# Performance work log

Hardware: AMD Instinct MI355X
Metric: run time of the kernel (lower is better)

The kernel has to match this reference:

```python
import jax, jax.numpy as jnp
import numpy as np

B_, DIM, HEADS, RES = 2, 288, 12, 32
# per-branch (D_sp, H_sp, W_sp) from idx permutation of split_size=[2,2,4]
WINS = ((2, 2, 4), (2, 2, 4), (2, 4, 2))
POS_DIM = ((DIM // 3) // 4) // 4  # = 6
HB = HEADS // 3  # heads per branch = 4


def _rel_tables(Dsp, Hsp, Wsp):
    d = np.arange(1 - Dsp, Dsp); h = np.arange(1 - Hsp, Hsp); w = np.arange(1 - Wsp, Wsp)
    biases = np.stack(np.meshgrid(d, h, w, indexing='ij')).reshape(3, -1).T.astype(np.float32)
    c = np.stack(np.meshgrid(np.arange(Dsp), np.arange(Hsp), np.arange(Wsp), indexing='ij')).reshape(3, -1)
    rel = (c[:, :, None] - c[:, None, :]).transpose(1, 2, 0).astype(np.int64)
    rel[..., 0] += Dsp - 1; rel[..., 1] += Hsp - 1; rel[..., 2] += Wsp - 1
    rel[..., 0] *= (2 * Hsp - 1) * (2 * Wsp - 1); rel[..., 1] *= 2 * Wsp - 1
    return biases, rel.sum(-1).astype(np.int32)


def _ln(x, g, b):
    m = x.mean(-1, keepdims=True)
    v = jnp.mean((x - m) ** 2, axis=-1, keepdims=True)
    return (x - m) * jax.lax.rsqrt(v + 1e-5) * g + b


def setup_inputs() -> dict:
    key = jax.random.key(0)
    ks = jax.random.split(key, 10)
    C, P, L = DIM, POS_DIM, RES ** 3
    s = 0.02
    x = jax.random.normal(ks[0], (B_, L, C), jnp.float32)
    w_qkv = jax.random.normal(ks[1], (C, 3 * C), jnp.float32) * s
    w_proj = jax.random.normal(ks[2], (C, C), jnp.float32) * s
    b_proj = jnp.zeros((C,), jnp.float32)
    conv_w = jax.random.normal(ks[3], (C, 1, 3, 3, 3), jnp.float32) * s  # depthwise OIDHW
    conv_b = jnp.zeros((C,), jnp.float32)
    pos_proj_w = jax.random.normal(ks[4], (3, 3, P), jnp.float32) * s
    pos_proj_b = jnp.zeros((3, P), jnp.float32)
    ln1_g = jnp.ones((3, P)); ln1_b = jnp.zeros((3, P))
    lin1_w = jax.random.normal(ks[5], (3, P, P), jnp.float32) * s; lin1_b = jnp.zeros((3, P))
    ln2_g = jnp.ones((3, P)); ln2_b = jnp.zeros((3, P))
    lin2_w = jax.random.normal(ks[6], (3, P, P), jnp.float32) * s; lin2_b = jnp.zeros((3, P))
    ln3_g = jnp.ones((3, P)); ln3_b = jnp.zeros((3, P))
    lin3_w = jax.random.normal(ks[7], (3, P, HB), jnp.float32) * s; lin3_b = jnp.zeros((3, HB))
    tabs = [_rel_tables(*w) for w in WINS]
    rpe_biases = jnp.asarray(np.stack([t[0] for t in tabs]))  # (3, 63, 3)
    rel_index = jnp.asarray(np.stack([t[1] for t in tabs]))   # (3, 16, 16)
    return {'x': x, 'D': RES, 'H': RES, 'W': RES, 'w_qkv': w_qkv, 'w_proj': w_proj,
            'b_proj': b_proj, 'conv_w': conv_w, 'conv_b': conv_b,
            'pos_proj_w': pos_proj_w, 'pos_proj_b': pos_proj_b,
            'ln1_g': ln1_g, 'ln1_b': ln1_b, 'lin1_w': lin1_w, 'lin1_b': lin1_b,
            'ln2_g': ln2_g, 'ln2_b': ln2_b, 'lin2_w': lin2_w, 'lin2_b': lin2_b,
            'ln3_g': ln3_g, 'ln3_b': ln3_b, 'lin3_w': lin3_w, 'lin3_b': lin3_b,
            'rpe_biases': rpe_biases, 'rel_index': rel_index}


def reference(x, D, H, W, w_qkv, w_proj, b_proj, conv_w, conv_b,
              pos_proj_w, pos_proj_b, ln1_g, ln1_b, lin1_w, lin1_b,
              ln2_g, ln2_b, lin2_w, lin2_b, ln3_g, ln3_b, lin3_w, lin3_b,
              rpe_biases, rel_index):
    B, L, C = x.shape
    C3 = C // 3
    hd = C3 // HB
    scale = hd ** -0.5
    qkv = (x @ w_qkv).reshape(B, L, 3, C).transpose(2, 0, 1, 3)  # (3, B, L, C)
    outs = []
    for bi, (Dsp, Hsp, Wsp) in enumerate(WINS):
        N = Dsp * Hsp * Wsp
        lo, hi = bi * C3, (bi + 1) * C3

        def to_win(t):
            # (B, L, C3) -> windows (B', HB, N, hd)
            t = t.reshape(B, D // Dsp, Dsp, H // Hsp, Hsp, W // Wsp, Wsp, C3)
            t = t.transpose(0, 1, 3, 5, 2, 4, 6, 7).reshape(-1, N, HB, hd)
            return t.transpose(0, 2, 1, 3)

        q = to_win(qkv[0, :, :, lo:hi]) * scale
        k = to_win(qkv[1, :, :, lo:hi])
        v = to_win(qkv[2, :, :, lo:hi])
        # dynamic relative position bias MLP (residual=False path)
        p = rpe_biases[bi] @ pos_proj_w[bi] + pos_proj_b[bi]
        p = jax.nn.relu(_ln(p, ln1_g[bi], ln1_b[bi])) @ lin1_w[bi] + lin1_b[bi]
        p = jax.nn.relu(_ln(p, ln2_g[bi], ln2_b[bi])) @ lin2_w[bi] + lin2_b[bi]
        p = jax.nn.relu(_ln(p, ln3_g[bi], ln3_b[bi])) @ lin3_w[bi] + lin3_b[bi]  # (T, HB)
        bias = p[rel_index[bi].reshape(-1)].reshape(N, N, HB).transpose(2, 0, 1)  # (HB, N, N)
        attn = jax.nn.softmax(jnp.einsum('whnd,whmd->whnm', q, k) + bias[None], axis=-1)
        o = jnp.einsum('whnm,whmd->whnd', attn, v)
        o = o.transpose(0, 2, 1, 3).reshape(B, D // Dsp, H // Hsp, W // Wsp, Dsp, Hsp, Wsp, C3)
        o = o.transpose(0, 1, 4, 2, 5, 3, 6, 7).reshape(B, D, H, W, C3)
        outs.append(o)
    att = jnp.concatenate(outs, axis=-1).reshape(B, L, C)
    # locally-enhanced branch: depthwise 3x3x3 conv over v
    vimg = qkv[2].reshape(B, D, H, W, C).transpose(0, 4, 1, 2, 3)
    lcm = jax.lax.conv_general_dilated(vimg, conv_w, (1, 1, 1), 'SAME',
                                       dimension_numbers=('NCDHW', 'OIDHW', 'NCDHW'),
                                       feature_group_count=C)
    lcm = (lcm + conv_b[None, :, None, None, None]).transpose(0, 2, 3, 4, 1).reshape(B, L, C)
    return (att + lcm) @ w_proj + b_proj
```

## Files before the change

### kernel.cpp

```cpp
#include <hip/hip_runtime.h>
#include <hip/hip_bf16.h>
#include <math.h>

#define BATCH 2
#define RES   32
#define LTOK  32768
#define CDIM  288
#define NQKV  864
#define MROWS 65536

typedef unsigned short u16;
typedef u16   u16x4 __attribute__((ext_vector_type(4)));
typedef short s16x8 __attribute__((ext_vector_type(8)));
typedef float f32x4 __attribute__((ext_vector_type(4)));

__device__ __forceinline__ u16 f2bf(float f) {
  union { __hip_bfloat16 h; u16 u; } x;
  x.h = __float2bfloat16(f);
  return x.u;
}
__device__ __forceinline__ float bf2f(u16 u) {
  union { u16 u; __hip_bfloat16 h; } x;
  x.u = u;
  return __bfloat162float(x.h);
}
__device__ __forceinline__ float bflo(unsigned u) {
  union { unsigned u; float f; } x; x.u = u << 16; return x.f;
}
__device__ __forceinline__ float bfhi(unsigned u) {
  union { unsigned u; float f; } x; x.u = u & 0xffff0000u; return x.f;
}

#define ASYNC16(gsrc, ldst)                                                        \
  __builtin_amdgcn_global_load_lds(                                                \
      (const __attribute__((address_space(1))) void*)(gsrc),                       \
      (__attribute__((address_space(3))) void*)(ldst), 16, 0, 0)

__global__ __launch_bounds__(256) void transpose_cvt(
    const float* __restrict__ w, u16* __restrict__ wt, int K, int N) {
  int o = blockIdx.x * 256 + threadIdx.x;
  if (o >= N * K) return;
  int n = o / K, k = o - n * K;
  wt[o] = f2bf(w[(size_t)k * N + n]);
}

__global__ __launch_bounds__(256) void conv_w_kmajor(
    const float* __restrict__ cw, float* __restrict__ wck) {
  int o = blockIdx.x * 256 + threadIdx.x;
  if (o >= 27 * 288) return;
  int k = o / 288, c = o - k * 288;
  wck[o] = cw[c * 27 + k];
}

template <bool BF16OUT, bool ABF16>
__global__ __launch_bounds__(512) void gemm_stream(
    const void* __restrict__ Ax, const u16* __restrict__ Bt,
    const float* __restrict__ bias, void* __restrict__ out, int N) {
  __shared__ __align__(16) u16 lds[36864];
  const int bm = blockIdx.x * 64;
  const int tid = threadIdx.x;
  const int lane = tid & 63, wave = tid >> 6;
  const int m16 = lane & 15, kq = lane >> 4;
  const int wm = (wave >> 1) * 16, wn = (wave & 1) * 16;
  const int NC = N >> 5;

  if (ABF16) {
    const u16* Ab = (const u16*)Ax;
    for (int g = wave; g < 36; g += 8)
      ASYNC16(Ab + (size_t)(bm + lane) * 288 + g * 8, &lds[g * 512]);
  } else {
    const float* Af = (const float*)Ax;
#pragma unroll
    for (int p = 0; p < 9; p++) {
      int s = p * 512 + tid;
      int g2 = s >> 7, r2 = (s & 127) >> 1, half = s & 1;
      float4 v = *(const float4*)(Af + (size_t)(bm + r2) * 288 + g2 * 8 + half * 4);
      u16x4 pk;
      pk[0] = f2bf(v.x); pk[1] = f2bf(v.y); pk[2] = f2bf(v.z); pk[3] = f2bf(v.w);
      *(u16x4*)&lds[g2 * 512 + r2 * 8 + half * 4] = pk;
    }
  }
  {
    const int r = lane & 31, gh = lane >> 5;
    for (int gp = wave; gp < 18; gp += 8)
      ASYNC16(Bt + (size_t)r * 288 + (gp * 2 + gh) * 8, &lds[18432 + gp * 512]);
  }
  asm volatile("s_waitcnt vmcnt(0) lgkmcnt(0)" ::: "memory");
  __builtin_amdgcn_s_barrier();

  int buf = 0;
  for (int c = 0; c < NC; c++) {
    if (c + 1 < NC) {
      const u16* Bc = Bt + (size_t)(c + 1) * 32 * 288;
      const int r = lane & 31, gh = lane >> 5;
      const int bb0 = 18432 + (buf ^ 1) * 9216;
      for (int gp = wave; gp < 18; gp += 8)
        ASYNC16(Bc + (size_t)r * 288 + (gp * 2 + gh) * 8, &lds[bb0 + gp * 512]);
    }
    __builtin_amdgcn_sched_barrier(0);

    f32x4 acc = {0.f, 0.f, 0.f, 0.f};
    const u16* bb = &lds[18432 + buf * 9216];
#pragma unroll
    for (int ks = 0; ks < 9; ks++) {
      const int g = ks * 4 + kq;
      s16x8 af = *(const s16x8*)&lds[g * 512 + (wm + m16) * 8];
      s16x8 bf = *(const s16x8*)&bb[g * 256 + (wn + m16) * 8];
      acc = __builtin_amdgcn_mfma_f32_16x16x32_bf16(af, bf, acc, 0, 0, 0);
    }
    const int col = (c << 5) + wn + m16;
    const size_t r0 = (size_t)(bm + wm + kq * 4);
    if (BF16OUT) {
      u16* op = (u16*)out;
#pragma unroll
      for (int r = 0; r < 4; r++) op[(r0 + r) * N + col] = f2bf(acc[r]);
    } else {
      const float bv = bias ? bias[col] : 0.f;
      float* op = (float*)out;
#pragma unroll
      for (int r = 0; r < 4; r++) op[(r0 + r) * N + col] = acc[r] + bv;
    }
    if (c + 1 < NC) {
      asm volatile("s_waitcnt vmcnt(4)" ::: "memory");
      __builtin_amdgcn_s_barrier();
    }
    buf ^= 1;
  }
}

__device__ __forceinline__ void ln_relu6(const float* x, float* o,
                                         const float* g, const float* b) {
  float m = 0.f;
#pragma unroll
  for (int i = 0; i < 6; i++) m += x[i];
  m *= (1.f / 6.f);
  float v = 0.f;
#pragma unroll
  for (int i = 0; i < 6; i++) { float d = x[i] - m; v += d * d; }
  v *= (1.f / 6.f);
  float r = rsqrtf(v + 1e-5f);
#pragma unroll
  for (int i = 0; i < 6; i++) {
    float t = (x[i] - m) * r * g[i] + b[i];
    o[i] = t > 0.f ? t : 0.f;
  }
}

__global__ __launch_bounds__(256) void rpe_mlp(
    const float* __restrict__ rpe, const float* __restrict__ pw, const float* __restrict__ pb,
    const float* __restrict__ g1, const float* __restrict__ b1,
    const float* __restrict__ w1, const float* __restrict__ bb1,
    const float* __restrict__ g2, const float* __restrict__ b2,
    const float* __restrict__ w2, const float* __restrict__ bb2,
    const float* __restrict__ g3, const float* __restrict__ b3,
    const float* __restrict__ w3, const float* __restrict__ bb3,
    float* __restrict__ ptab) {
  int t = blockIdx.x * blockDim.x + threadIdx.x;
  if (t >= 3 * 63) return;
  int bi = t / 63, row = t % 63;
  float p[6], q[6];
#pragma unroll
  for (int j = 0; j < 6; j++) {
    float s = pb[bi * 6 + j];
#pragma unroll
    for (int i = 0; i < 3; i++) s += rpe[(bi * 63 + row) * 3 + i] * pw[(bi * 3 + i) * 6 + j];
    p[j] = s;
  }
  ln_relu6(p, q, g1 + bi * 6, b1 + bi * 6);
#pragma unroll
  for (int j = 0; j < 6; j++) {
    float s = bb1[bi * 6 + j];
#pragma unroll
    for (int i = 0; i < 6; i++) s += q[i] * w1[(bi * 6 + i) * 6 + j];
    p[j] = s;
  }
  ln_relu6(p, q, g2 + bi * 6, b2 + bi * 6);
#pragma unroll
  for (int j = 0; j < 6; j++) {
    float s = bb2[bi * 6 + j];
#pragma unroll
    for (int i = 0; i < 6; i++) s += q[i] * w2[(bi * 6 + i) * 6 + j];
    p[j] = s;
  }
  ln_relu6(p, q, g3 + bi * 6, b3 + bi * 6);
#pragma unroll
  for (int h = 0; h < 4; h++) {
    float s = bb3[bi * 4 + h];
#pragma unroll
    for (int i = 0; i < 6; i++) s += q[i] * w3[(bi * 6 + i) * 4 + h];
    ptab[(bi * 63 + row) * 4 + h] = s;
  }
}

__global__ __launch_bounds__(64) void attn_kernel(
    const u16* __restrict__ qkv, const float* __restrict__ ptab,
    const int* __restrict__ rel, float* __restrict__ y) {
  const int bi = blockIdx.y;
  const int wsh = (bi == 2) ? 1 : 2;
  const int hsh = (bi == 2) ? 2 : 1;
  const int Wm1 = (1 << wsh) - 1, Hm1 = (1 << hsh) - 1;
  const int nW = RES >> wsh, nH = RES >> hsh;
  const int wid = blockIdx.x;
  const int b = wid >> 11;
  const int r_ = wid & 2047;
  const int w0 = r_ % nW;
  const int r2 = r_ / nW;
  const int h0 = r2 % nH;
  const int d0 = r2 / nH;

  __shared__ __align__(16) u16 sq[16 * 40];
  __shared__ __align__(16) u16 sk[16 * 40];
  __shared__ __align__(16) u16 svt[32 * 40];
  __shared__ __align__(16) u16 sps[16 * 40];

  const int lane = threadIdx.x;
  const int m16 = lane & 15, q4 = lane >> 4;

  {
    uint4 z = make_uint4(0u, 0u, 0u, 0u);
#pragma unroll
    for (int i = lane; i < 80; i += 64) {
      *(uint4*)&sq[i * 8] = z;
      *(uint4*)&sk[i * 8] = z;
    }
#pragma unroll
    for (int i = lane; i < 160; i += 64)
      *(uint4*)&svt[i * 8] = z;
  }
  __syncthreads();

  int rv[4];
#pragma unroll
  for (int r = 0; r < 4; r++) rv[r] = rel[(bi * 16 + q4 * 4 + r) * 16 + m16];

  size_t ybase[4];
#pragma unroll
  for (int r = 0; r < 4; r++) {
    int n = q4 * 4 + r;
    int dd = n >> 3, hh2 = (n >> wsh) & Hm1, ww = n & Wm1;
    int l = ((d0 * 2 + dd) * RES + ((h0 << hsh) + hh2)) * RES + ((w0 << wsh) + ww);
    ybase[r] = (size_t)(b * LTOK + l) * CDIM + bi * 96;
  }

  const float scale = 0.20412414523193154f;

  for (int hd = 0; hd < 4; hd++) {
#pragma unroll
    for (int it = 0; it < 2; it++) {
      int idx = it * 64 + lane;
      if (idx < 96) {
        int n = idx / 6, c4 = idx - n * 6, ch = c4 * 4;
        int dd = n >> 3, hh2 = (n >> wsh) & Hm1, ww = n & Wm1;
        int l = ((d0 * 2 + dd) * RES + ((h0 << hsh) + hh2)) * RES + ((w0 << wsh) + ww);
        size_t base = (size_t)(b * LTOK + l) * NQKV + bi * 96 + hd * 24 + ch;
        u16x4 qv = *(const u16x4*)(qkv + base);
        u16x4 kv = *(const u16x4*)(qkv + base + 288);
        u16x4 vv = *(const u16x4*)(qkv + base + 576);
        *(u16x4*)&sq[n * 40 + ch] = qv;
        *(u16x4*)&sk[n * 40 + ch] = kv;
#pragma unroll
        for (int j = 0; j < 4; j++) {
          svt[(ch + j) * 40 + n] = vv[j];
          svt[(ch + j) * 40 + 16 + n] = vv[j];
        }
      }
    }
    __syncthreads();

    s16x8 af = *(const s16x8*)&sq[m16 * 40 + q4 * 8];
    s16x8 bf = *(const s16x8*)&sk[m16 * 40 + q4 * 8];
    f32x4 sc = __builtin_amdgcn_mfma_f32_16x16x32_bf16(af, bf, (f32x4){0.f, 0.f, 0.f, 0.f}, 0, 0, 0);

    float inv[4];
#pragma unroll
    for (int r = 0; r < 4; r++) {
      float s = sc[r] * scale + ptab[(size_t)(bi * 63 + rv[r]) * 4 + hd];
      float mx = s;
#pragma unroll
      for (int msk = 1; msk <= 8; msk <<= 1) mx = fmaxf(mx, __shfl_xor(mx, msk));
      float e = expf(s - mx);
      float sum = e;
#pragma unroll
      for (int msk = 1; msk <= 8; msk <<= 1) sum += __shfl_xor(sum, msk);
      inv[r] = 1.f / sum;
      u16 hi = f2bf(e);
      float lo = e - bf2f(hi);
      sps[(q4 * 4 + r) * 40 + m16] = hi;
      sps[(q4 * 4 + r) * 40 + 16 + m16] = f2bf(lo);
    }
    __syncthreads();

    s16x8 pa = *(const s16x8*)&sps[m16 * 40 + q4 * 8];
    s16x8 v1 = *(const s16x8*)&svt[m16 * 40 + q4 * 8];
    s16x8 v2 = *(const s16x8*)&svt[(16 + m16) * 40 + q4 * 8];
    f32x4 o1 = __builtin_amdgcn_mfma_f32_16x16x32_bf16(pa, v1, (f32x4){0.f, 0.f, 0.f, 0.f}, 0, 0, 0);
    f32x4 o2 = __builtin_amdgcn_mfma_f32_16x16x32_bf16(pa, v2, (f32x4){0.f, 0.f, 0.f, 0.f}, 0, 0, 0);

#pragma unroll
    for (int r = 0; r < 4; r++) {
      float* yp = y + ybase[r] + hd * 24;
      yp[m16] = o1[r] * inv[r];
      if (m16 < 8) yp[16 + m16] = o2[r] * inv[r];
    }
    __syncthreads();
  }
}

template <bool BF16OUT>
__global__ __launch_bounds__(512, 4) void conv_tile_kernel(
    const u16* __restrict__ qkv, const float* __restrict__ wck,
    const float* __restrict__ cb, float* __restrict__ y, u16* __restrict__ ybf) {
  __shared__ __align__(16) u16 vs[1000 * 40];
  const int tid = threadIdx.x;
  const int bx = blockIdx.x;
  const int c0 = blockIdx.y * 32;
  const int b = bx >> 6;
  const int t = bx & 63;
  const int td = (t >> 4) * 8, th = ((t >> 2) & 3) * 8, tw = (t & 3) * 8;

#pragma unroll
  for (int p = 0; p < 8; p++) {
    int idx = p * 512 + tid;
    if (idx < 4000) {
      int tok = idx >> 2, chunk = idx & 3;
      int dz = tok / 100, rem = tok - dz * 100;
      int hz = rem / 10, wz = rem - hz * 10;
      int d = td + dz - 1, h = th + hz - 1, w = tw + wz - 1;
      uint4 v = make_uint4(0u, 0u, 0u, 0u);
      if ((unsigned)d < 32u && (unsigned)h < 32u && (unsigned)w < 32u)
        v = *(const uint4*)(qkv +
              ((size_t)(b * LTOK + ((d * 32 + h) * 32 + w))) * NQKV + 576 + c0 + chunk * 8);
      *(uint4*)&vs[tok * 40 + chunk * 8] = v;
    }
  }
  __syncthreads();

  const int d = tid >> 6, h = (tid >> 3) & 7, w = tid & 7;
  float acc[32];
#pragma unroll
  for (int c = 0; c < 32; c++) acc[c] = cb[c0 + c];

  for (int kd = 0; kd < 3; kd++) {
#pragma unroll
    for (int kh = 0; kh < 3; kh++) {
#pragma unroll
      for (int kw = 0; kw < 3; kw++) {
        const int k = kd * 9 + kh * 3 + kw;
        const float* wk = wck + k * 288 + c0;
        const u16* p0 = &vs[(((d + kd) * 100 + (h + kh) * 10) + (w + kw)) * 40];
#pragma unroll
        for (int cq = 0; cq < 4; cq++) {
          uint4 v0 = *(const uint4*)(p0 + cq * 8);
          const unsigned* u0 = (const unsigned*)&v0;
#pragma unroll
          for (int j = 0; j < 4; j++) {
            const int ce = cq * 8 + j * 2;
            acc[ce]     += bflo(u0[j]) * wk[ce];
            acc[ce + 1] += bfhi(u0[j]) * wk[ce + 1];
          }
        }
      }
    }
  }

  const int tt = b * LTOK + ((td + d) * 32 + (th + h)) * 32 + (tw + w);

  if (BF16OUT) {
    const float4* yp = (const float4*)&y[(size_t)tt * CDIM + c0];
    unsigned pk[16];
#pragma unroll
    for (int q = 0; q < 8; q++) {
      float4 cur = yp[q];
      float va = cur.x + acc[q * 4],     vb = cur.y + acc[q * 4 + 1];
      float vc = cur.z + acc[q * 4 + 2], vd = cur.w + acc[q * 4 + 3];
      pk[q * 2]     = (unsigned)f2bf(va) | ((unsigned)f2bf(vb) << 16);
      pk[q * 2 + 1] = (unsigned)f2bf(vc) | ((unsigned)f2bf(vd) << 16);
    }
    uint4* op = (uint4*)(ybf + (size_t)tt * CDIM + c0);
#pragma unroll
    for (int q = 0; q < 4; q++) op[q] = ((const uint4*)pk)[q];
  } else {
    float4* yp = (float4*)&y[(size_t)tt * CDIM + c0];
#pragma unroll
    for (int q = 0; q < 8; q++) {
      float4 cur = yp[q];
      cur.x += acc[q * 4];     cur.y += acc[q * 4 + 1];
      cur.z += acc[q * 4 + 2]; cur.w += acc[q * 4 + 3];
      yp[q] = cur;
    }
  }
}

extern "C" void kernel_launch(void* const* d_in, const int* in_sizes, int n_in,
                              void* d_out, int out_size, void* d_ws, size_t ws_size,
                              hipStream_t stream) {
  const float* x      = (const float*)d_in[0];
  const float* w_qkv  = (const float*)d_in[4];
  const float* w_proj = (const float*)d_in[5];
  const float* b_proj = (const float*)d_in[6];
  const float* conv_w = (const float*)d_in[7];
  const float* conv_b = (const float*)d_in[8];
  const float* pos_w  = (const float*)d_in[9];
  const float* pos_b  = (const float*)d_in[10];
  const float* ln1_g  = (const float*)d_in[11];
  const float* ln1_b  = (const float*)d_in[12];
  const float* lin1_w = (const float*)d_in[13];
  const float* lin1_b = (const float*)d_in[14];
  const float* ln2_g  = (const float*)d_in[15];
  const float* ln2_b  = (const float*)d_in[16];
  const float* lin2_w = (const float*)d_in[17];
  const float* lin2_b = (const float*)d_in[18];
  const float* ln3_g  = (const float*)d_in[19];
  const float* ln3_b  = (const float*)d_in[20];
  const float* lin3_w = (const float*)d_in[21];
  const float* lin3_b = (const float*)d_in[22];
  const float* rpe    = (const float*)d_in[23];
  const int*   rel    = (const int*)d_in[24];
  float* out = (float*)d_out;

  const size_t Q = (size_t)MROWS * NQKV * sizeof(u16);
  u16* qkv   = (u16*)d_ws;
  u16* wqt   = (u16*)((char*)d_ws + Q);
  u16* wpt   = (u16*)((char*)d_ws + Q + 497664);
  float* ptab  = (float*)((char*)d_ws + Q + 497664 + 165888);
  float* wck   = (float*)((char*)d_ws + Q + 497664 + 165888 + 3024);

  const size_t yoff = (Q + 497664 + 165888 + 3024 + 31104 + 255) & ~(size_t)255;
  const size_t ybf_bytes = (size_t)MROWS * CDIM * sizeof(u16);
  const bool big = ws_size >= yoff + ybf_bytes;
  u16* ybf = (u16*)((char*)d_ws + yoff);

  transpose_cvt<<<(NQKV * CDIM + 255) / 256, 256, 0, stream>>>(w_qkv, wqt, CDIM, NQKV);
  transpose_cvt<<<(CDIM * CDIM + 255) / 256, 256, 0, stream>>>(w_proj, wpt, CDIM, CDIM);
  conv_w_kmajor<<<(27 * 288 + 255) / 256, 256, 0, stream>>>(conv_w, wck);
  gemm_stream<true, false><<<MROWS / 64, 512, 0, stream>>>(x, wqt, nullptr, qkv, NQKV);
  rpe_mlp<<<1, 256, 0, stream>>>(rpe, pos_w, pos_b, ln1_g, ln1_b, lin1_w, lin1_b,
                                 ln2_g, ln2_b, lin2_w, lin2_b, ln3_g, ln3_b,
                                 lin3_w, lin3_b, ptab);
  attn_kernel<<<dim3(4096, 3), 64, 0, stream>>>(qkv, ptab, rel, out);
  if (big) {
    conv_tile_kernel<true><<<dim3(128, 9), 512, 0, stream>>>(qkv, wck, conv_b, out, ybf);
    gemm_stream<false, true><<<MROWS / 64, 512, 0, stream>>>(ybf, wpt, b_proj, out, CDIM);
  } else {
    conv_tile_kernel<false><<<dim3(128, 9), 512, 0, stream>>>(qkv, wck, conv_b, out, nullptr);
    gemm_stream<false, false><<<MROWS / 64, 512, 0, stream>>>(out, wpt, b_proj, out, CDIM);
  }
}
```

Before: 422.8 us.

## Keep A tile in LDS, stream B from global per wave; pack 4 attention windows per block

The GEMM now keeps the 64-row A tile resident in LDS while each of 4 waves owns whole 32-column chunks. Each wave reads B fragments directly from global/L2 and computes a 64x32 output block with 8 accumulators, which removes the double-buffered B staging and per-chunk barriers. The attention kernel packs four windows per 256-thread block, each wave with private LDS. It drops all __syncthreads, zeroes only the padding, and widens qkv loads to 16 bytes. The risks are more global B traffic and register pressure in the GEMM, and that the attention kernel relies on wave-level LDS ordering without barriers.

```diff
diff --git a/kernel.cpp b/kernel.cpp
--- a/kernel.cpp
+++ b/kernel.cpp
@@ -53,78 +53,81 @@
 }
 
 template <bool BF16OUT, bool ABF16>
-__global__ __launch_bounds__(512) void gemm_stream(
+__global__ __launch_bounds__(256, 4) void gemm_ares(
     const void* __restrict__ Ax, const u16* __restrict__ Bt,
     const float* __restrict__ bias, void* __restrict__ out, int N) {
-  __shared__ __align__(16) u16 lds[36864];
+  __shared__ __align__(16) u16 As[18432];
   const int bm = blockIdx.x * 64;
   const int tid = threadIdx.x;
   const int lane = tid & 63, wave = tid >> 6;
   const int m16 = lane & 15, kq = lane >> 4;
-  const int wm = (wave >> 1) * 16, wn = (wave & 1) * 16;
   const int NC = N >> 5;
 
   if (ABF16) {
     const u16* Ab = (const u16*)Ax;
-    for (int g = wave; g < 36; g += 8)
-      ASYNC16(Ab + (size_t)(bm + lane) * 288 + g * 8, &lds[g * 512]);
+    for (int g = wave; g < 36; g += 4)
+      ASYNC16(Ab + (size_t)(bm + lane) * 288 + g * 8, &As[g * 512]);
+    asm volatile("s_waitcnt vmcnt(0)" ::: "memory");
   } else {
     const float* Af = (const float*)Ax;
 #pragma unroll
-    for (int p = 0; p < 9; p++) {
-      int s = p * 512 + tid;
+    for (int p = 0; p < 18; p++) {
+      int s = p * 256 + tid;
       int g2 = s >> 7, r2 = (s & 127) >> 1, half = s & 1;
       float4 v = *(const float4*)(Af + (size_t)(bm + r2) * 288 + g2 * 8 + half * 4);
       u16x4 pk;
       pk[0] = f2bf(v.x); pk[1] = f2bf(v.y); pk[2] = f2bf(v.z); pk[3] = f2bf(v.w);
-      *(u16x4*)&lds[g2 * 512 + r2 * 8 + half * 4] = pk;
-    }
-  }
-  {
-    const int r = lane & 31, gh = lane >> 5;
-    for (int gp = wave; gp < 18; gp += 8)
-      ASYNC16(Bt + (size_t)r * 288 + (gp * 2 + gh) * 8, &lds[18432 + gp * 512]);
-  }
-  asm volatile("s_waitcnt vmcnt(0) lgkmcnt(0)" ::: "memory");
-  __builtin_amdgcn_s_barrier();
-
-  int buf = 0;
-  for (int c = 0; c < NC; c++) {
-    if (c + 1 < NC) {
-      const u16* Bc = Bt + (size_t)(c + 1) * 32 * 288;
-      const int r = lane & 31, gh = lane >> 5;
-      const int bb0 = 18432 + (buf ^ 1) * 9216;
-      for (int gp = wave; gp < 18; gp += 8)
-        ASYNC16(Bc + (size_t)r * 288 + (gp * 2 + gh) * 8, &lds[bb0 + gp * 512]);
-    }
-    __builtin_amdgcn_sched_barrier(0);
-
-    f32x4 acc = {0.f, 0.f, 0.f, 0.f};
-    const u16* bb = &lds[18432 + buf * 9216];
+      *(u16x4*)&As[g2 * 512 + r2 * 8 + half * 4] = pk;
+    }
+  }
+  __syncthreads();
+
+  for (int c = wave; c < NC; c += 4) {
+    const u16* Bc = Bt + ((size_t)c << 5) * 288;
+    f32x4 acc[4][2];
+#pragma unroll
+    for (int mi = 0; mi < 4; mi++)
+#pragma unroll
+      for (int ni = 0; ni < 2; ni++) acc[mi][ni] = (f32x4){0.f, 0.f, 0.f, 0.f};
+
 #pragma unroll
     for (int ks = 0; ks < 9; ks++) {
+      s16x8 bf[2];
+#pragma unroll
+      for (int ni = 0; ni < 2; ni++)
+        bf[ni] = *(const s16x8*)(Bc + (size_t)(ni * 16 + m16) * 288 + ks * 32 + kq * 8);
       const int g = ks * 4 + kq;
-      s16x8 af = *(const s16x8*)&lds[g * 512 + (wm + m16) * 8];
-      s16x8 bf = *(const s16x8*)&bb[g * 256 + (wn + m16) * 8];
-      acc = __builtin_amdgcn_mfma_f32_16x16x32_bf16(af, bf, acc, 0, 0, 0);
-    }
-    const int col = (c << 5) + wn + m16;
-    const size_t r0 = (size_t)(bm + wm + kq * 4);
+#pragma unroll
+      for (int mi = 0; mi < 4; mi++) {
+        s16x8 af = *(const s16x8*)&As[g * 512 + (mi * 16 + m16) * 8];
+#pragma unroll
+        for (int ni = 0; ni < 2; ni++)
+          acc[mi][ni] = __builtin_amdgcn_mfma_f32_16x16x32_bf16(af, bf[ni], acc[mi][ni], 0, 0, 0);
+      }
+    }
     if (BF16OUT) {
       u16* op = (u16*)out;
 #pragma unroll
-      for (int r = 0; r < 4; r++) op[(r0 + r) * N + col] = f2bf(acc[r]);
+      for (int mi = 0; mi < 4; mi++)
+#pragma unroll
+        for (int ni = 0; ni < 2; ni++)
+#pragma unroll
+          for (int r = 0; r < 4; r++)
+            op[(size_t)(bm + mi * 16 + kq * 4 + r) * N + (c << 5) + ni * 16 + m16] =
+                f2bf(acc[mi][ni][r]);
     } else {
-      const float bv = bias ? bias[col] : 0.f;
       float* op = (float*)out;
 #pragma unroll
-      for (int r = 0; r < 4; r++) op[(r0 + r) * N + col] = acc[r] + bv;
-    }
-    if (c + 1 < NC) {
-      asm volatile("s_waitcnt vmcnt(4)" ::: "memory");
-      __builtin_amdgcn_s_barrier();
-    }
-    buf ^= 1;
+      for (int ni = 0; ni < 2; ni++) {
+        const int col = (c << 5) + ni * 16 + m16;
+        const float bv = bias ? bias[col] : 0.f;
+#pragma unroll
+        for (int mi = 0; mi < 4; mi++)
+#pragma unroll
+          for (int r = 0; r < 4; r++)
+            op[(size_t)(bm + mi * 16 + kq * 4 + r) * N + col] = acc[mi][ni][r] + bv;
+      }
+    }
   }
 }
 
@@ -192,15 +195,22 @@
   }
 }
 
-__global__ __launch_bounds__(64) void attn_kernel(
+__global__ __launch_bounds__(256) void attn_kernel(
     const u16* __restrict__ qkv, const float* __restrict__ ptab,
     const int* __restrict__ rel, float* __restrict__ y) {
+  __shared__ __align__(16) u16 sq[4][640];
+  __shared__ __align__(16) u16 sk[4][640];
+  __shared__ __align__(16) u16 svt[4][1280];
+  __shared__ __align__(16) u16 sps[4][640];
+
   const int bi = blockIdx.y;
   const int wsh = (bi == 2) ? 1 : 2;
   const int hsh = (bi == 2) ? 2 : 1;
   const int Wm1 = (1 << wsh) - 1, Hm1 = (1 << hsh) - 1;
   const int nW = RES >> wsh, nH = RES >> hsh;
-  const int wid = blockIdx.x;
+  const int tid = threadIdx.x;
+  const int wv = tid >> 6, lane = tid & 63;
+  const int wid = blockIdx.x * 4 + wv;
   const int b = wid >> 11;
   const int r_ = wid & 2047;
   const int w0 = r_ % nW;
@@ -208,26 +218,23 @@
   const int h0 = r2 % nH;
   const int d0 = r2 / nH;
 
-  __shared__ __align__(16) u16 sq[16 * 40];
-  __shared__ __align__(16) u16 sk[16 * 40];
-  __shared__ __align__(16) u16 svt[32 * 40];
-  __shared__ __align__(16) u16 sps[16 * 40];
-
-  const int lane = threadIdx.x;
+  u16* q_  = sq[wv];
+  u16* k_  = sk[wv];
+  u16* vt_ = svt[wv];
+  u16* ps_ = sps[wv];
   const int m16 = lane & 15, q4 = lane >> 4;
 
   {
     uint4 z = make_uint4(0u, 0u, 0u, 0u);
-#pragma unroll
-    for (int i = lane; i < 80; i += 64) {
-      *(uint4*)&sq[i * 8] = z;
-      *(uint4*)&sk[i * 8] = z;
-    }
-#pragma unroll
-    for (int i = lane; i < 160; i += 64)
-      *(uint4*)&svt[i * 8] = z;
-  }
-  __syncthreads();
+    if (lane < 16) {
+      *(uint4*)&q_[lane * 40 + 24] = z;
+      *(uint4*)&k_[lane * 40 + 24] = z;
+    }
+    if (lane < 40) {
+      int row = 24 + lane / 5, ch = (lane % 5) * 8;
+      *(uint4*)&vt_[row * 40 + ch] = z;
+    }
+  }
 
   int rv[4];
 #pragma unroll
@@ -245,30 +252,26 @@
   const float scale = 0.20412414523193154f;
 
   for (int hd = 0; hd < 4; hd++) {
-#pragma unroll
-    for (int it = 0; it < 2; it++) {
-      int idx = it * 64 + lane;
-      if (idx < 96) {
-        int n = idx / 6, c4 = idx - n * 6, ch = c4 * 4;
-        int dd = n >> 3, hh2 = (n >> wsh) & Hm1, ww = n & Wm1;
-        int l = ((d0 * 2 + dd) * RES + ((h0 << hsh) + hh2)) * RES + ((w0 << wsh) + ww);
-        size_t base = (size_t)(b * LTOK + l) * NQKV + bi * 96 + hd * 24 + ch;
-        u16x4 qv = *(const u16x4*)(qkv + base);
-        u16x4 kv = *(const u16x4*)(qkv + base + 288);
-        u16x4 vv = *(const u16x4*)(qkv + base + 576);
-        *(u16x4*)&sq[n * 40 + ch] = qv;
-        *(u16x4*)&sk[n * 40 + ch] = kv;
-#pragma unroll
-        for (int j = 0; j < 4; j++) {
-          svt[(ch + j) * 40 + n] = vv[j];
-          svt[(ch + j) * 40 + 16 + n] = vv[j];
-        }
+    if (lane < 48) {
+      int n = lane / 3, ch = (lane % 3) * 8;
+      int dd = n >> 3, hh2 = (n >> wsh) & Hm1, ww = n & Wm1;
+      int l = ((d0 * 2 + dd) * RES + ((h0 << hsh) + hh2)) * RES + ((w0 << wsh) + ww);
+      size_t base = (size_t)(b * LTOK + l) * NQKV + bi * 96 + hd * 24 + ch;
+      uint4 qv = *(const uint4*)(qkv + base);
+      uint4 kv = *(const uint4*)(qkv + base + 288);
+      uint4 vv = *(const uint4*)(qkv + base + 576);
+      *(uint4*)&q_[n * 40 + ch] = qv;
+      *(uint4*)&k_[n * 40 + ch] = kv;
+      const u16* vp = (const u16*)&vv;
+#pragma unroll
+      for (int j = 0; j < 8; j++) {
+        vt_[(ch + j) * 40 + n] = vp[j];
+        vt_[(ch + j) * 40 + 16 + n] = vp[j];
       }
     }
-    __syncthreads();
-
-    s16x8 af = *(const s16x8*)&sq[m16 * 40 + q4 * 8];
-    s16x8 bf = *(const s16x8*)&sk[m16 * 40 + q4 * 8];
+
+    s16x8 af = *(const s16x8*)&q_[m16 * 40 + q4 * 8];
+    s16x8 bf = *(const s16x8*)&k_[m16 * 40 + q4 * 8];
     f32x4 sc = __builtin_amdgcn_mfma_f32_16x16x32_bf16(af, bf, (f32x4){0.f, 0.f, 0.f, 0.f}, 0, 0, 0);
 
     float inv[4];
@@ -285,14 +288,13 @@
       inv[r] = 1.f / sum;
       u16 hi = f2bf(e);
       float lo = e - bf2f(hi);
-      sps[(q4 * 4 + r) * 40 + m16] = hi;
-      sps[(q4 * 4 + r) * 40 + 16 + m16] = f2bf(lo);
-    }
-    __syncthreads();
-
-    s16x8 pa = *(const s16x8*)&sps[m16 * 40 + q4 * 8];
-    s16x8 v1 = *(const s16x8*)&svt[m16 * 40 + q4 * 8];
-    s16x8 v2 = *(const s16x8*)&svt[(16 + m16) * 40 + q4 * 8];
+      ps_[(q4 * 4 + r) * 40 + m16] = hi;
+      ps_[(q4 * 4 + r) * 40 + 16 + m16] = f2bf(lo);
+    }
+
+    s16x8 pa = *(const s16x8*)&ps_[m16 * 40 + q4 * 8];
+    s16x8 v1 = *(const s16x8*)&vt_[m16 * 40 + q4 * 8];
+    s16x8 v2 = *(const s16x8*)&vt_[(16 + m16) * 40 + q4 * 8];
     f32x4 o1 = __builtin_amdgcn_mfma_f32_16x16x32_bf16(pa, v1, (f32x4){0.f, 0.f, 0.f, 0.f}, 0, 0, 0);
     f32x4 o2 = __builtin_amdgcn_mfma_f32_16x16x32_bf16(pa, v2, (f32x4){0.f, 0.f, 0.f, 0.f}, 0, 0, 0);
 
@@ -302,7 +304,6 @@
       yp[m16] = o1[r] * inv[r];
       if (m16 < 8) yp[16 + m16] = o2[r] * inv[r];
     }
-    __syncthreads();
   }
 }
 
@@ -433,16 +434,16 @@
   transpose_cvt<<<(NQKV * CDIM + 255) / 256, 256, 0, stream>>>(w_qkv, wqt, CDIM, NQKV);
   transpose_cvt<<<(CDIM * CDIM + 255) / 256, 256, 0, stream>>>(w_proj, wpt, CDIM, CDIM);
   conv_w_kmajor<<<(27 * 288 + 255) / 256, 256, 0, stream>>>(conv_w, wck);
-  gemm_stream<true, false><<<MROWS / 64, 512, 0, stream>>>(x, wqt, nullptr, qkv, NQKV);
+  gemm_ares<true, false><<<MROWS / 64, 256, 0, stream>>>(x, wqt, nullptr, qkv, NQKV);
   rpe_mlp<<<1, 256, 0, stream>>>(rpe, pos_w, pos_b, ln1_g, ln1_b, lin1_w, lin1_b,
                                  ln2_g, ln2_b, lin2_w, lin2_b, ln3_g, ln3_b,
                                  lin3_w, lin3_b, ptab);
-  attn_kernel<<<dim3(4096, 3), 64, 0, stream>>>(qkv, ptab, rel, out);
+  attn_kernel<<<dim3(1024, 3), 256, 0, stream>>>(qkv, ptab, rel, out);
   if (big) {
     conv_tile_kernel<true><<<dim3(128, 9), 512, 0, stream>>>(qkv, wck, conv_b, out, ybf);
-    gemm_stream<false, true><<<MROWS / 64, 512, 0, stream>>>(ybf, wpt, b_proj, out, CDIM);
+    gemm_ares<false, true><<<MROWS / 64, 256, 0, stream>>>(ybf, wpt, b_proj, out, CDIM);
   } else {
     conv_tile_kernel<false><<<dim3(128, 9), 512, 0, stream>>>(qkv, wck, conv_b, out, nullptr);
-    gemm_stream<false, false><<<MROWS / 64, 512, 0, stream>>>(out, wpt, b_proj, out, CDIM);
-  }
-}
+    gemm_ares<false, false><<<MROWS / 64, 256, 0, stream>>>(out, wpt, b_proj, out, CDIM);
+  }
+}
```

Result: slower. 619.8 us (+46.6%).
